# Kernel optimization log

Measured on AMD Instinct MI355X. Metric: run time of the kernel, lower is better.

The kernel has to match this reference:

```python
import jax, jax.numpy as jnp
import numpy as np

H = 4096
W = 4096
N_CELLS = H * W
ITERATIONS = 16


def setup_inputs() -> dict:
    key = jax.random.key(0)
    k1, k2 = jax.random.split(key)
    runoff = jax.random.uniform(k1, (H, W), dtype=jnp.float32)
    # each cell's downstream receiver cell (flat index into H*W grid)
    flow_idx = jax.random.randint(k2, (N_CELLS,), 0, N_CELLS, dtype=jnp.int32)
    return {
        "runoff_generated": runoff,
        "flow_direction_indices": flow_idx,
        "iterations": ITERATIONS,
    }


def reference(runoff_generated, flow_direction_indices, iterations):
    h, w = runoff_generated.shape
    current = runoff_generated.reshape(-1)   # (N,)
    accumulated = current                      # clone of initial flow

    def step(carry, _):
        accum, cur = carry
        # scatter-add: every cell pushes its current flow downstream
        accum = accum.at[flow_direction_indices].add(cur)
        cur = accum - cur
        return (accum, cur), None

    (accumulated, _), _ = jax.lax.scan(step, (accumulated, current), None, length=iterations)
    return accumulated.reshape(h, w)
```

## Files before the change

### kernel.cpp

```cpp
#include <hip/hip_runtime.h>


#define N_CELLS (1 << 24)

#define BKT_BITS 14
#define NBKT (N_CELLS >> BKT_BITS)
#define DPB (1 << BKT_BITS)
#define BKT_MASK (DPB - 1)
#define IDX_MASK (N_CELLS - 1)
#define G1 256
#define EDGES_PER_WG (N_CELLS / G1)
#define BT 1024

typedef unsigned uv4 __attribute__((ext_vector_type(4)));
typedef float fv4 __attribute__((ext_vector_type(4)));
typedef unsigned long long u64;

__device__ __align__(16) unsigned g_T[2][NBKT * G1];
__device__ __align__(16) unsigned g_bktcnt[2][NBKT];
__device__ __align__(16) unsigned g_S[2][NBKT + 4];
__device__ __align__(16) uint2 g_rec[N_CELLS];
__device__ __align__(16) int g_idx2[N_CELLS];
__device__ __align__(16) int g_idx4[N_CELLS];
__device__ __align__(16) float gB1[N_CELLS];
__device__ __align__(16) float gB2[N_CELLS];
__device__ __align__(16) float gB3[N_CELLS];
__device__ __align__(16) float gH[N_CELLS];

__global__ void compose_idx(const int* __restrict__ ext, int mode) {
    const int* __restrict__ a = mode ? g_idx2 : ext;
    int* __restrict__ o = mode ? g_idx4 : g_idx2;
    int i = (blockIdx.x * 256 + threadIdx.x) * 4;
    int4 v = *reinterpret_cast<const int4*>(a + i);
    int4 r;
    r.x = a[v.x & IDX_MASK];
    r.y = a[v.y & IDX_MASK];
    r.z = a[v.z & IDX_MASK];
    r.w = a[v.w & IDX_MASK];
    *reinterpret_cast<int4*>(o + i) = r;
}

__global__ void __launch_bounds__(BT) b1_count(const int* __restrict__ ext, int set) {
    const int* __restrict__ idx = set ? g_idx4 : ext;
    __shared__ unsigned h[NBKT];
    int t = threadIdx.x;
    h[t] = 0u;
    __syncthreads();
    const uv4* p = reinterpret_cast<const uv4*>(idx) + (size_t)blockIdx.x * (EDGES_PER_WG / 4);
    for (int k = 0; k < EDGES_PER_WG / 4 / BT; ++k) {
        uv4 v = __builtin_nontemporal_load(&p[k * BT + t]);
        atomicAdd(&h[(v.x & IDX_MASK) >> BKT_BITS], 1u);
        atomicAdd(&h[(v.y & IDX_MASK) >> BKT_BITS], 1u);
        atomicAdd(&h[(v.z & IDX_MASK) >> BKT_BITS], 1u);
        atomicAdd(&h[(v.w & IDX_MASK) >> BKT_BITS], 1u);
    }
    __syncthreads();
    g_T[set][(size_t)t * G1 + blockIdx.x] = h[t];
}

__global__ void s1_sums(int set) {
    __shared__ unsigned sd[256];
    int t = threadIdx.x;
    sd[t] = g_T[set][(size_t)blockIdx.x * G1 + t];
    __syncthreads();
    for (int off = 128; off > 0; off >>= 1) {
        if (t < off) sd[t] += sd[t + off];
        __syncthreads();
    }
    if (t == 0) g_bktcnt[set][blockIdx.x] = sd[0];
}

__global__ void s2_scan(int set) {
    __shared__ unsigned s[256];
    int t = threadIdx.x;
    uint4 v = reinterpret_cast<const uint4*>(g_bktcnt[set])[t];
    unsigned local = v.x + v.y + v.z + v.w;
    s[t] = local;
    __syncthreads();
    for (int off = 1; off < 256; off <<= 1) {
        unsigned add = (t >= off) ? s[t - off] : 0u;
        __syncthreads();
        s[t] += add;
        __syncthreads();
    }
    unsigned run = s[t] - local;
    uint4 o;
    o.x = run; run += v.x;
    o.y = run; run += v.y;
    o.z = run; run += v.z;
    o.w = run;
    reinterpret_cast<uint4*>(g_S[set])[t] = o;
    if (t == 0) g_S[set][NBKT] = (unsigned)N_CELLS;
}

__global__ void s3_offsets(int set) {
    __shared__ unsigned s[256];
    int t = threadIdx.x;
    unsigned v = g_T[set][(size_t)blockIdx.x * G1 + t];
    s[t] = v;
    __syncthreads();
    for (int off = 1; off < 256; off <<= 1) {
        unsigned add = (t >= off) ? s[t - off] : 0u;
        __syncthreads();
        s[t] += add;
        __syncthreads();
    }
    g_T[set][(size_t)blockIdx.x * G1 + t] = g_S[set][blockIdx.x] + s[t] - v;
}

__device__ __forceinline__ float* sel_buf(int which, const float* r, float* dout) {
    switch (which) {
        case 0: return (float*)r;
        case 1: return gB1;
        case 2: return gB2;
        case 3: return gB3;
        case 4: return gH;
        default: return dout;
    }
}

__global__ void __launch_bounds__(BT) route_op(const float* __restrict__ rin,
                                               float* __restrict__ dout,
                                               const int* __restrict__ ext,
                                               int ct_sel, int set) {
    const int* __restrict__ idx = set ? g_idx4 : ext;
    const float* __restrict__ ct = sel_buf(ct_sel, rin, dout);
    __shared__ unsigned cur[NBKT];
    int t = threadIdx.x;
    cur[t] = g_T[set][(size_t)t * G1 + blockIdx.x];
    __syncthreads();
    const uv4* ip = reinterpret_cast<const uv4*>(idx) + (size_t)blockIdx.x * (EDGES_PER_WG / 4);
    const fv4* cp = reinterpret_cast<const fv4*>(ct) + (size_t)blockIdx.x * (EDGES_PER_WG / 4);
    for (int k = 0; k < EDGES_PER_WG / 4 / BT; ++k) {
        uv4 v = __builtin_nontemporal_load(&ip[k * BT + t]);
        fv4 c = __builtin_nontemporal_load(&cp[k * BT + t]);
        unsigned e, p;
        e = v.x & IDX_MASK; p = atomicAdd(&cur[e >> BKT_BITS], 1u) & IDX_MASK;
        g_rec[p] = make_uint2(__float_as_uint(c.x), e & BKT_MASK);
        e = v.y & IDX_MASK; p = atomicAdd(&cur[e >> BKT_BITS], 1u) & IDX_MASK;
        g_rec[p] = make_uint2(__float_as_uint(c.y), e & BKT_MASK);
        e = v.z & IDX_MASK; p = atomicAdd(&cur[e >> BKT_BITS], 1u) & IDX_MASK;
        g_rec[p] = make_uint2(__float_as_uint(c.z), e & BKT_MASK);
        e = v.w & IDX_MASK; p = atomicAdd(&cur[e >> BKT_BITS], 1u) & IDX_MASK;
        g_rec[p] = make_uint2(__float_as_uint(c.w), e & BKT_MASK);
    }
}

__global__ void __launch_bounds__(512) acc_op(const float* __restrict__ rin,
                                              float* __restrict__ dout,
                                              int out_sel, int set, int fuse,
                                              float a0, float a1, float a2, float a3) {
    __shared__ float acc[DPB];
    int t = threadIdx.x;
    unsigned b = blockIdx.x;
    float* __restrict__ out = sel_buf(out_sel, rin, dout);
    unsigned base = g_S[set][b];
    unsigned end = g_S[set][b + 1];
    if (end > (unsigned)N_CELLS) end = (unsigned)N_CELLS;
    if (base > end) base = end;
    fv4* acc4 = reinterpret_cast<fv4*>(acc);
    fv4 z = (fv4)(0.0f);
    for (int k = 0; k < DPB / 4 / 512; ++k) acc4[k * 512 + t] = z;
    __syncthreads();
    const u64* __restrict__ rec = reinterpret_cast<const u64*>(g_rec);
    unsigned e = base + t;
    for (; e + 1536 < end; e += 2048) {
        u64 q0 = __builtin_nontemporal_load(&rec[e]);
        u64 q1 = __builtin_nontemporal_load(&rec[e + 512]);
        u64 q2 = __builtin_nontemporal_load(&rec[e + 1024]);
        u64 q3 = __builtin_nontemporal_load(&rec[e + 1536]);
        atomicAdd(&acc[(unsigned)(q0 >> 32) & BKT_MASK], __uint_as_float((unsigned)q0));
        atomicAdd(&acc[(unsigned)(q1 >> 32) & BKT_MASK], __uint_as_float((unsigned)q1));
        atomicAdd(&acc[(unsigned)(q2 >> 32) & BKT_MASK], __uint_as_float((unsigned)q2));
        atomicAdd(&acc[(unsigned)(q3 >> 32) & BKT_MASK], __uint_as_float((unsigned)q3));
    }
    for (; e < end; e += 512) {
        u64 q = __builtin_nontemporal_load(&rec[e]);
        atomicAdd(&acc[(unsigned)(q >> 32) & BKT_MASK], __uint_as_float((unsigned)q));
    }
    __syncthreads();
    size_t rowbase = (size_t)b * (DPB / 4);
    fv4* out4 = reinterpret_cast<fv4*>(out) + rowbase;
    if (fuse) {
        const fv4* r4 = reinterpret_cast<const fv4*>(rin) + rowbase;
        const fv4* p1 = reinterpret_cast<const fv4*>(gB1) + rowbase;
        const fv4* p2 = reinterpret_cast<const fv4*>(gB2) + rowbase;
        const fv4* p3 = reinterpret_cast<const fv4*>(gB3) + rowbase;
        for (int k = 0; k < DPB / 4 / 512; ++k) {
            int j = k * 512 + t;
            fv4 a = acc4[j];
            fv4 x = __builtin_nontemporal_load(&r4[j]);
            fv4 y = __builtin_nontemporal_load(&p1[j]);
            fv4 u = __builtin_nontemporal_load(&p2[j]);
            fv4 w = __builtin_nontemporal_load(&p3[j]);
            a += a0 * x + a1 * y + a2 * u + a3 * w;
            __builtin_nontemporal_store(a, &out4[j]);
        }
    } else {
        for (int k = 0; k < DPB / 4 / 512; ++k) {
            int j = k * 512 + t;
            __builtin_nontemporal_store(acc4[j], &out4[j]);
        }
    }
}

extern "C" void kernel_launch(void* const* d_in, const int* in_sizes, int n_in,
                              void* d_out, int out_size, void* d_ws, size_t ws_size,
                              hipStream_t stream) {
    const int* idx = (const int*)d_in[1];
    const float* r = (const float*)d_in[0];
    float* out = (float*)d_out;

    b1_count<<<G1, BT, 0, stream>>>(idx, 0);
    s1_sums<<<NBKT, 256, 0, stream>>>(0);
    s2_scan<<<1, 256, 0, stream>>>(0);
    s3_offsets<<<NBKT, 256, 0, stream>>>(0);

    compose_idx<<<N_CELLS / 4 / 256, 256, 0, stream>>>(idx, 0);
    compose_idx<<<N_CELLS / 4 / 256, 256, 0, stream>>>(idx, 1);
    b1_count<<<G1, BT, 0, stream>>>(idx, 1);
    s1_sums<<<NBKT, 256, 0, stream>>>(1);
    s2_scan<<<1, 256, 0, stream>>>(1);
    s3_offsets<<<NBKT, 256, 0, stream>>>(1);

    route_op<<<G1, BT, 0, stream>>>(r, out, idx, 0, 0);
    acc_op<<<NBKT, 512, 0, stream>>>(r, out, 1, 0, 0, 0.f, 0.f, 0.f, 0.f);
    route_op<<<G1, BT, 0, stream>>>(r, out, idx, 1, 0);
    acc_op<<<NBKT, 512, 0, stream>>>(r, out, 2, 0, 0, 0.f, 0.f, 0.f, 0.f);
    route_op<<<G1, BT, 0, stream>>>(r, out, idx, 2, 0);
    acc_op<<<NBKT, 512, 0, stream>>>(r, out, 3, 0, 0, 0.f, 0.f, 0.f, 0.f);

    route_op<<<G1, BT, 0, stream>>>(r, out, idx, 0, 1);
    acc_op<<<NBKT, 512, 0, stream>>>(r, out, 4, 1, 1, 91.f, 14.f, 15.f, 1.f);
    route_op<<<G1, BT, 0, stream>>>(r, out, idx, 4, 1);
    acc_op<<<NBKT, 512, 0, stream>>>(r, out, 5, 1, 1, 495.f, 220.f, 286.f, 78.f);
    route_op<<<G1, BT, 0, stream>>>(r, out, idx, 5, 1);
    acc_op<<<NBKT, 512, 0, stream>>>(r, out, 4, 1, 1, 210.f, 252.f, 462.f, 330.f);
    route_op<<<G1, BT, 0, stream>>>(r, out, idx, 4, 1);
    acc_op<<<NBKT, 512, 0, stream>>>(r, out, 5, 1, 1, 1.f, 8.f, 36.f, 84.f);
}
```

Measured before the change: 3.133 ms.

## Split single-pass 1024-way bucket scatter into two-pass 32x32 radix partition

Replaces the one-pass scatter of edge records into 1024 destination buckets with two passes: first partition into 32 super-buckets, then redistribute each super-bucket region into 32 sub-buckets, using new offset tables. The aim is better write locality, since each pass writes to far fewer concurrent output streams, which should reduce scattered, partially filled cache-line writes. In exchange, every routing step now makes an extra full read and write of the 8-byte record array plus an additional kernel launch.

```diff
diff --git a/kernel.cpp b/kernel.cpp
--- a/kernel.cpp
+++ b/kernel.cpp
@@ -8,9 +8,11 @@
 #define DPB (1 << BKT_BITS)
 #define BKT_MASK (DPB - 1)
 #define IDX_MASK (N_CELLS - 1)
+#define NSUP 32
+#define SUP_SHIFT 19
 #define G1 256
-#define EDGES_PER_WG (N_CELLS / G1)
 #define BT 1024
+#define EPW (N_CELLS / G1)
 
 typedef unsigned uv4 __attribute__((ext_vector_type(4)));
 typedef float fv4 __attribute__((ext_vector_type(4)));
@@ -19,6 +21,9 @@
 __device__ __align__(16) unsigned g_T[2][NBKT * G1];
 __device__ __align__(16) unsigned g_bktcnt[2][NBKT];
 __device__ __align__(16) unsigned g_S[2][NBKT + 4];
+__device__ __align__(16) unsigned g_off1[2][NSUP * G1];
+__device__ __align__(16) unsigned g_off2[2][NBKT * 8];
+__device__ __align__(16) uint2 g_tmp[N_CELLS];
 __device__ __align__(16) uint2 g_rec[N_CELLS];
 __device__ __align__(16) int g_idx2[N_CELLS];
 __device__ __align__(16) int g_idx4[N_CELLS];
@@ -26,6 +31,17 @@
 __device__ __align__(16) float gB2[N_CELLS];
 __device__ __align__(16) float gB3[N_CELLS];
 __device__ __align__(16) float gH[N_CELLS];
+
+__device__ __forceinline__ float* sel_buf(int which, const float* r, float* dout) {
+    switch (which) {
+        case 0: return (float*)r;
+        case 1: return gB1;
+        case 2: return gB2;
+        case 3: return gB3;
+        case 4: return gH;
+        default: return dout;
+    }
+}
 
 __global__ void compose_idx(const int* __restrict__ ext, int mode) {
     const int* __restrict__ a = mode ? g_idx2 : ext;
@@ -46,8 +62,8 @@
     int t = threadIdx.x;
     h[t] = 0u;
     __syncthreads();
-    const uv4* p = reinterpret_cast<const uv4*>(idx) + (size_t)blockIdx.x * (EDGES_PER_WG / 4);
-    for (int k = 0; k < EDGES_PER_WG / 4 / BT; ++k) {
+    const uv4* p = reinterpret_cast<const uv4*>(idx) + (size_t)blockIdx.x * (EPW / 4);
+    for (int k = 0; k < EPW / 4 / BT; ++k) {
         uv4 v = __builtin_nontemporal_load(&p[k * BT + t]);
         atomicAdd(&h[(v.x & IDX_MASK) >> BKT_BITS], 1u);
         atomicAdd(&h[(v.y & IDX_MASK) >> BKT_BITS], 1u);
@@ -93,56 +109,104 @@
     if (t == 0) g_S[set][NBKT] = (unsigned)N_CELLS;
 }
 
-__global__ void s3_offsets(int set) {
-    __shared__ unsigned s[256];
-    int t = threadIdx.x;
-    unsigned v = g_T[set][(size_t)blockIdx.x * G1 + t];
-    s[t] = v;
-    __syncthreads();
-    for (int off = 1; off < 256; off <<= 1) {
-        unsigned add = (t >= off) ? s[t - off] : 0u;
-        __syncthreads();
-        s[t] += add;
-        __syncthreads();
-    }
-    g_T[set][(size_t)blockIdx.x * G1 + t] = g_S[set][blockIdx.x] + s[t] - v;
-}
-
-__device__ __forceinline__ float* sel_buf(int which, const float* r, float* dout) {
-    switch (which) {
-        case 0: return (float*)r;
-        case 1: return gB1;
-        case 2: return gB2;
-        case 3: return gB3;
-        case 4: return gH;
-        default: return dout;
-    }
-}
-
-__global__ void __launch_bounds__(BT) route_op(const float* __restrict__ rin,
-                                               float* __restrict__ dout,
-                                               const int* __restrict__ ext,
-                                               int ct_sel, int set) {
+__global__ void d_off1(int set) {
+    __shared__ unsigned sc[G1];
+    int w = threadIdx.x;
+    unsigned s = blockIdx.x;
+    unsigned c = 0u;
+    for (int j = 0; j < NBKT / NSUP; ++j)
+        c += g_T[set][(size_t)(s * (NBKT / NSUP) + j) * G1 + w];
+    sc[w] = c;
+    __syncthreads();
+    for (int off = 1; off < G1; off <<= 1) {
+        unsigned add = (w >= off) ? sc[w - off] : 0u;
+        __syncthreads();
+        sc[w] += add;
+        __syncthreads();
+    }
+    g_off1[set][(size_t)s * G1 + w] = g_S[set][s * (NBKT / NSUP)] + sc[w] - c;
+}
+
+__global__ void d_off2(int set) {
+    __shared__ unsigned sd[256];
+    int t = threadIdx.x;
+    unsigned b = blockIdx.x;
+    sd[t] = g_T[set][(size_t)b * G1 + t];
+    __syncthreads();
+    for (int off = 16; off > 0; off >>= 1) {
+        if ((t & 31) < off) sd[t] += sd[t + off];
+        __syncthreads();
+    }
+    if (t == 0) {
+        unsigned run = g_S[set][b];
+        for (int g = 0; g < 8; ++g) {
+            g_off2[set][(size_t)b * 8 + g] = run;
+            run += sd[g * 32];
+        }
+    }
+}
+
+__global__ void __launch_bounds__(BT) route1(const float* __restrict__ rin,
+                                             float* __restrict__ dout,
+                                             const int* __restrict__ ext,
+                                             int ct_sel, int set) {
     const int* __restrict__ idx = set ? g_idx4 : ext;
     const float* __restrict__ ct = sel_buf(ct_sel, rin, dout);
-    __shared__ unsigned cur[NBKT];
-    int t = threadIdx.x;
-    cur[t] = g_T[set][(size_t)t * G1 + blockIdx.x];
-    __syncthreads();
-    const uv4* ip = reinterpret_cast<const uv4*>(idx) + (size_t)blockIdx.x * (EDGES_PER_WG / 4);
-    const fv4* cp = reinterpret_cast<const fv4*>(ct) + (size_t)blockIdx.x * (EDGES_PER_WG / 4);
-    for (int k = 0; k < EDGES_PER_WG / 4 / BT; ++k) {
+    __shared__ unsigned cur[NSUP];
+    int t = threadIdx.x;
+    if (t < NSUP) cur[t] = g_off1[set][(size_t)t * G1 + blockIdx.x];
+    __syncthreads();
+    const uv4* ip = reinterpret_cast<const uv4*>(idx) + (size_t)blockIdx.x * (EPW / 4);
+    const fv4* cp = reinterpret_cast<const fv4*>(ct) + (size_t)blockIdx.x * (EPW / 4);
+    for (int k = 0; k < EPW / 4 / BT; ++k) {
         uv4 v = __builtin_nontemporal_load(&ip[k * BT + t]);
         fv4 c = __builtin_nontemporal_load(&cp[k * BT + t]);
         unsigned e, p;
-        e = v.x & IDX_MASK; p = atomicAdd(&cur[e >> BKT_BITS], 1u) & IDX_MASK;
-        g_rec[p] = make_uint2(__float_as_uint(c.x), e & BKT_MASK);
-        e = v.y & IDX_MASK; p = atomicAdd(&cur[e >> BKT_BITS], 1u) & IDX_MASK;
-        g_rec[p] = make_uint2(__float_as_uint(c.y), e & BKT_MASK);
-        e = v.z & IDX_MASK; p = atomicAdd(&cur[e >> BKT_BITS], 1u) & IDX_MASK;
-        g_rec[p] = make_uint2(__float_as_uint(c.z), e & BKT_MASK);
-        e = v.w & IDX_MASK; p = atomicAdd(&cur[e >> BKT_BITS], 1u) & IDX_MASK;
-        g_rec[p] = make_uint2(__float_as_uint(c.w), e & BKT_MASK);
+        e = v.x & IDX_MASK; p = atomicAdd(&cur[e >> SUP_SHIFT], 1u) & IDX_MASK;
+        g_tmp[p] = make_uint2(__float_as_uint(c.x), e);
+        e = v.y & IDX_MASK; p = atomicAdd(&cur[e >> SUP_SHIFT], 1u) & IDX_MASK;
+        g_tmp[p] = make_uint2(__float_as_uint(c.y), e);
+        e = v.z & IDX_MASK; p = atomicAdd(&cur[e >> SUP_SHIFT], 1u) & IDX_MASK;
+        g_tmp[p] = make_uint2(__float_as_uint(c.z), e);
+        e = v.w & IDX_MASK; p = atomicAdd(&cur[e >> SUP_SHIFT], 1u) & IDX_MASK;
+        g_tmp[p] = make_uint2(__float_as_uint(c.w), e);
+    }
+}
+
+__global__ void __launch_bounds__(BT) route2(int set) {
+    __shared__ unsigned cur[NSUP];
+    unsigned wg = blockIdx.x;
+    unsigned s = wg >> 3, g = wg & 7u;
+    int t = threadIdx.x;
+    if (t < NSUP) cur[t] = g_off2[set][(size_t)(s * NSUP + t) * 8 + g];
+    __syncthreads();
+    unsigned start = g_off1[set][(size_t)s * G1 + g * 32];
+    unsigned end = (g < 7u) ? g_off1[set][(size_t)s * G1 + (g + 1) * 32]
+                            : g_S[set][(s + 1) * NSUP];
+    if (start > end) start = end;
+    const u64* __restrict__ tmp = reinterpret_cast<const u64*>(g_tmp);
+    unsigned e = start + t;
+    for (; e + 3 * BT < end; e += 4 * BT) {
+        u64 q0 = __builtin_nontemporal_load(&tmp[e]);
+        u64 q1 = __builtin_nontemporal_load(&tmp[e + BT]);
+        u64 q2 = __builtin_nontemporal_load(&tmp[e + 2 * BT]);
+        u64 q3 = __builtin_nontemporal_load(&tmp[e + 3 * BT]);
+        unsigned d0 = (unsigned)(q0 >> 32), d1 = (unsigned)(q1 >> 32);
+        unsigned d2 = (unsigned)(q2 >> 32), d3 = (unsigned)(q3 >> 32);
+        unsigned p0 = atomicAdd(&cur[(d0 >> BKT_BITS) & 31u], 1u) & IDX_MASK;
+        unsigned p1 = atomicAdd(&cur[(d1 >> BKT_BITS) & 31u], 1u) & IDX_MASK;
+        unsigned p2 = atomicAdd(&cur[(d2 >> BKT_BITS) & 31u], 1u) & IDX_MASK;
+        unsigned p3 = atomicAdd(&cur[(d3 >> BKT_BITS) & 31u], 1u) & IDX_MASK;
+        g_rec[p0] = make_uint2((unsigned)q0, d0);
+        g_rec[p1] = make_uint2((unsigned)q1, d1);
+        g_rec[p2] = make_uint2((unsigned)q2, d2);
+        g_rec[p3] = make_uint2((unsigned)q3, d3);
+    }
+    for (; e < end; e += BT) {
+        u64 q = __builtin_nontemporal_load(&tmp[e]);
+        unsigned d = (unsigned)(q >> 32);
+        unsigned p = atomicAdd(&cur[(d >> BKT_BITS) & 31u], 1u) & IDX_MASK;
+        g_rec[p] = make_uint2((unsigned)q, d);
     }
 }
 
@@ -214,28 +278,37 @@
     b1_count<<<G1, BT, 0, stream>>>(idx, 0);
     s1_sums<<<NBKT, 256, 0, stream>>>(0);
     s2_scan<<<1, 256, 0, stream>>>(0);
-    s3_offsets<<<NBKT, 256, 0, stream>>>(0);
+    d_off1<<<NSUP, G1, 0, stream>>>(0);
+    d_off2<<<NBKT, 256, 0, stream>>>(0);
 
     compose_idx<<<N_CELLS / 4 / 256, 256, 0, stream>>>(idx, 0);
     compose_idx<<<N_CELLS / 4 / 256, 256, 0, stream>>>(idx, 1);
     b1_count<<<G1, BT, 0, stream>>>(idx, 1);
     s1_sums<<<NBKT, 256, 0, stream>>>(1);
     s2_scan<<<1, 256, 0, stream>>>(1);
-    s3_offsets<<<NBKT, 256, 0, stream>>>(1);
-
-    route_op<<<G1, BT, 0, stream>>>(r, out, idx, 0, 0);
+    d_off1<<<NSUP, G1, 0, stream>>>(1);
+    d_off2<<<NBKT, 256, 0, stream>>>(1);
+
+    route1<<<G1, BT, 0, stream>>>(r, out, idx, 0, 0);
+    route2<<<G1, BT, 0, stream>>>(0);
     acc_op<<<NBKT, 512, 0, stream>>>(r, out, 1, 0, 0, 0.f, 0.f, 0.f, 0.f);
-    route_op<<<G1, BT, 0, stream>>>(r, out, idx, 1, 0);
+    route1<<<G1, BT, 0, stream>>>(r, out, idx, 1, 0);
+    route2<<<G1, BT, 0, stream>>>(0);
     acc_op<<<NBKT, 512, 0, stream>>>(r, out, 2, 0, 0, 0.f, 0.f, 0.f, 0.f);
-    route_op<<<G1, BT, 0, stream>>>(r, out, idx, 2, 0);
+    route1<<<G1, BT, 0, stream>>>(r, out, idx, 2, 0);
+    route2<<<G1, BT, 0, stream>>>(0);
     acc_op<<<NBKT, 512, 0, stream>>>(r, out, 3, 0, 0, 0.f, 0.f, 0.f, 0.f);
 
-    route_op<<<G1, BT, 0, stream>>>(r, out, idx, 0, 1);
+    route1<<<G1, BT, 0, stream>>>(r, out, idx, 0, 1);
+    route2<<<G1, BT, 0, stream>>>(1);
     acc_op<<<NBKT, 512, 0, stream>>>(r, out, 4, 1, 1, 91.f, 14.f, 15.f, 1.f);
-    route_op<<<G1, BT, 0, stream>>>(r, out, idx, 4, 1);
+    route1<<<G1, BT, 0, stream>>>(r, out, idx, 4, 1);
+    route2<<<G1, BT, 0, stream>>>(1);
     acc_op<<<NBKT, 512, 0, stream>>>(r, out, 5, 1, 1, 495.f, 220.f, 286.f, 78.f);
-    route_op<<<G1, BT, 0, stream>>>(r, out, idx, 5, 1);
+    route1<<<G1, BT, 0, stream>>>(r, out, idx, 5, 1);
+    route2<<<G1, BT, 0, stream>>>(1);
     acc_op<<<NBKT, 512, 0, stream>>>(r, out, 4, 1, 1, 210.f, 252.f, 462.f, 330.f);
-    route_op<<<G1, BT, 0, stream>>>(r, out, idx, 4, 1);
+    route1<<<G1, BT, 0, stream>>>(r, out, idx, 4, 1);
+    route2<<<G1, BT, 0, stream>>>(1);
     acc_op<<<NBKT, 512, 0, stream>>>(r, out, 5, 1, 1, 1.f, 8.f, 36.f, 84.f);
 }
```

Result: faster. 2.579 ms (-17.7%).
